# Optimization experiments

Measured on AMD Instinct MI355X. Metric: run time of the kernel, lower is better.

Reference implementation:

```python
import jax, jax.numpy as jnp
import numpy as np

DECAY = 0.99
EPS = 1e-05


def setup_inputs() -> dict:
    key = jax.random.key(0)
    k1, k2 = jax.random.split(key)
    N, D, K = 262144, 32, 1024
    z = jax.random.normal(k1, (N, D), dtype=jnp.float32)
    # xavier_normal_ on (K, D): std = sqrt(2 / (K + D))
    std = float(np.sqrt(2.0 / (K + D)))
    embedding = jax.random.normal(k2, (K, D), dtype=jnp.float32) * std
    embed_avg = embedding  # buffer initialized as a clone of the codebook
    cluster_size = jnp.ones((K,), dtype=jnp.float32)
    return {"z": z, "embedding": embedding, "embed_avg": embed_avg,
            "cluster_size": cluster_size}


def reference(z, embedding, embed_avg, cluster_size):
    n_embed, embed_dim = embedding.shape
    # squared euclidean cdist: ||z||^2 + ||e||^2 - 2 z e^T  -> [N, K]
    d = (jnp.sum(z * z, axis=1, keepdims=True)
         + jnp.sum(embedding * embedding, axis=1)
         - 2.0 * (z @ embedding.T))
    encoding_indices = jnp.argmin(d, axis=1)  # [N]
    # one-hot column sums via scatter-add (counts per code)
    counts = jnp.zeros((n_embed,), z.dtype).at[encoding_indices].add(1.0)
    unused_codes = jnp.sum(counts == 0)
    # embedding gather
    z_q = embedding[encoding_indices]  # [N, D]
    # EMA scatter-add update (training branch, use_ema=True)
    embed_sum = jnp.zeros_like(embedding).at[encoding_indices].add(z)  # [K, D]
    cluster_size_new = DECAY * cluster_size + (1.0 - DECAY) * counts
    embed_avg_new = DECAY * embed_avg + (1.0 - DECAY) * embed_sum
    n = jnp.sum(cluster_size_new)
    norm_w = n * (cluster_size_new + EPS) / (n + n_embed * EPS)  # Laplace smoothing
    embedding_new = embed_avg_new / norm_w[:, None]
    codebook_loss = jnp.float32(0.0)
    commitment_loss = jnp.mean((z - jax.lax.stop_gradient(z_q)) ** 2)
    # straight-through estimator
    z_q_out = z + jax.lax.stop_gradient(z_q - z)
    return (z_q_out, codebook_loss, commitment_loss, encoding_indices,
            unused_codes, embedding_new, cluster_size_new, embed_avg_new)
```

## Files before the change

### kernel.cpp

```cpp
#include <hip/hip_runtime.h>
#include <hip/hip_bf16.h>
#include <float.h>

#define DIM 32
#define KCODES 1024
#define NROWS 262144

#define O_ZQ   0
#define O_CB   8388608
#define O_CL   8388609
#define O_IDX  8388610
#define O_UN   8650754
#define O_EMB  8650755
#define O_CS   8683523
#define O_EA   8684547

#define W_PCNT 0
#define W_PSUM 262144
#define W_PCOM 8650752
#define W_NORM 8651008
#define W_ZZH  8652032
#define W_EEH  8914176
#define W_BF   8915200

typedef __attribute__((ext_vector_type(8))) short bf16x8;
typedef __attribute__((ext_vector_type(4))) float f32x4;

#define MFMA16 __builtin_amdgcn_mfma_f32_16x16x32_bf16

static __device__ __forceinline__ unsigned short f2bf(float x) {
    __hip_bfloat16 h = __float2bfloat16(x);
    return __builtin_bit_cast(unsigned short, h);
}
static __device__ __forceinline__ float bf2f(unsigned short u) {
    unsigned int v = ((unsigned int)u) << 16;
    return __builtin_bit_cast(float, v);
}
static __device__ __forceinline__ float pw8_sq(const float* x) {
    float w[32];
    #pragma unroll
    for (int i = 0; i < 32; ++i) w[i] = __fmul_rn(x[i], x[i]);
    float r[8];
    #pragma unroll
    for (int j = 0; j < 8; ++j) r[j] = ((w[j] + w[8 + j]) + w[16 + j]) + w[24 + j];
    return ((r[0] + r[1]) + (r[2] + r[3])) + ((r[4] + r[5]) + (r[6] + r[7]));
}

__global__ __launch_bounds__(256) void vq_prep_z(
    const float* __restrict__ z, float* __restrict__ ws)
{
    int row = blockIdx.x * 256 + threadIdx.x;
    float x[32];
    const float4* zg = (const float4*)(z + (size_t)row * DIM);
    #pragma unroll
    for (int q = 0; q < 8; ++q) {
        float4 v = zg[q];
        x[4*q] = v.x; x[4*q+1] = v.y; x[4*q+2] = v.z; x[4*q+3] = v.w;
    }
    ws[W_ZZH + row] = 0.5f * pw8_sq(x);
}

__global__ __launch_bounds__(256) void vq_prep_e(
    const float* __restrict__ emb, float* __restrict__ ws)
{
    int c = blockIdx.x * 256 + threadIdx.x;
    float x[32];
    const float4* eg = (const float4*)(emb + (size_t)c * DIM);
    #pragma unroll
    for (int q = 0; q < 8; ++q) {
        float4 v = eg[q];
        x[4*q] = v.x; x[4*q+1] = v.y; x[4*q+2] = v.z; x[4*q+3] = v.w;
    }
    ws[W_EEH + c] = 0.5f * pw8_sq(x);

    unsigned short hb[3][32];
    #pragma unroll
    for (int i = 0; i < 32; ++i) {
        float v = x[i];
        unsigned short h0 = f2bf(v); float f0 = bf2f(h0); float r1 = v - f0;
        unsigned short h1 = f2bf(r1); float f1 = bf2f(h1); float r2 = r1 - f1;
        unsigned short h2 = f2bf(r2);
        hb[0][i] = h0; hb[1][i] = h1; hb[2][i] = h2;
    }
    bf16x8* bf = (bf16x8*)(ws + W_BF);
    int kt = c >> 4, cl = c & 15;
    #pragma unroll
    for (int s = 0; s < 3; ++s) {
        #pragma unroll
        for (int j = 0; j < 4; ++j) {
            bf16x8 pk;
            #pragma unroll
            for (int e = 0; e < 8; ++e) pk[e] = (short)hb[s][j*8 + e];
            bf[(kt*3 + s)*64 + j*16 + cl] = pk;
        }
    }
}

__global__ __launch_bounds__(256, 4) void vq_argmin_mfma(
    const float* __restrict__ z, const float* __restrict__ wsc,
    float* __restrict__ out)
{
    __shared__ float eesh[1024];
    const int t = threadIdx.x;
    const int lane = t & 63, w = t >> 6;
    const int g = lane >> 4, lr = lane & 15;

    const bf16x8* bvG = (const bf16x8*)(wsc + W_BF);

    #pragma unroll
    for (int i = 0; i < 4; ++i) eesh[t + i * 256] = wsc[W_EEH + t + i * 256];

    const int rtbase = blockIdx.x * 16 + w * 4;
    bf16x8 zh[4], zm[4], zl[4];
    float zza[4][4];
    #pragma unroll
    for (int j = 0; j < 4; ++j) {
        const int rtg = rtbase + j;
        const float* zp = z + ((size_t)(rtg * 16 + lr)) * DIM + g * 8;
        float4 a4 = *(const float4*)zp, b4 = *(const float4*)(zp + 4);
        float xs[8] = {a4.x, a4.y, a4.z, a4.w, b4.x, b4.y, b4.z, b4.w};
        #pragma unroll
        for (int e = 0; e < 8; ++e) {
            float v = xs[e];
            unsigned short h0 = f2bf(v); float f0 = bf2f(h0); float r1 = v - f0;
            unsigned short h1 = f2bf(r1); float f1 = bf2f(h1); float r2 = r1 - f1;
            zh[j][e] = (short)h0; zm[j][e] = (short)h1; zl[j][e] = (short)f2bf(r2);
        }
        float4 zv = *(const float4*)(wsc + W_ZZH + rtg * 16 + g * 4);
        zza[j][0] = zv.x; zza[j][1] = zv.y; zza[j][2] = zv.z; zza[j][3] = zv.w;
    }

    unsigned int Bb[4][4]; int Kk[4][4];
    #pragma unroll
    for (int j = 0; j < 4; ++j)
        #pragma unroll
        for (int r = 0; r < 4; ++r) { Bb[j][r] = 0xFFFFFFFFu; Kk[j][r] = 0; }

    __syncthreads();

    #pragma unroll 2
    for (int kt = 0; kt < 64; ++kt) {
        bf16x8 eh = bvG[(kt * 3 + 0) * 64 + lane];
        bf16x8 em = bvG[(kt * 3 + 1) * 64 + lane];
        bf16x8 el = bvG[(kt * 3 + 2) * 64 + lane];
        float ee_l = eesh[kt * 16 + lr];
        int kge = kt * 16 + lr;
        #pragma unroll
        for (int j = 0; j < 4; ++j) {
            f32x4 a = {0.f, 0.f, 0.f, 0.f};
            a = MFMA16(zh[j], eh, a, 0, 0, 0);
            a = MFMA16(zh[j], em, a, 0, 0, 0);
            a = MFMA16(zm[j], eh, a, 0, 0, 0);
            a = MFMA16(zh[j], el, a, 0, 0, 0);
            a = MFMA16(zl[j], eh, a, 0, 0, 0);
            a = MFMA16(zm[j], em, a, 0, 0, 0);
            #pragma unroll
            for (int r = 0; r < 4; ++r) {
                float v = (zza[j][r] + ee_l) - a[r];
                unsigned int u = __builtin_bit_cast(unsigned int, v);
                bool tk = u < Bb[j][r];
                Bb[j][r] = tk ? u : Bb[j][r];
                Kk[j][r] = tk ? kge : Kk[j][r];
            }
        }
    }

    #pragma unroll
    for (int j = 0; j < 4; ++j) {
        const int rtg = rtbase + j;
        #pragma unroll
        for (int r = 0; r < 4; ++r) {
            unsigned int b0 = Bb[j][r]; int k0 = Kk[j][r];
            #pragma unroll
            for (int m = 1; m < 16; m <<= 1) {
                unsigned int ob = __shfl_xor((int)b0, m, 16); int ok = __shfl_xor(k0, m, 16);
                bool tk = (ob < b0) || (ob == b0 && ok < k0);
                b0 = tk ? ob : b0; k0 = tk ? ok : k0;
            }
            if (lr == 0) out[O_IDX + rtg * 16 + g * 4 + r] = (float)k0;
        }
    }
}

__global__ __launch_bounds__(1024) void vq_scatter(
    const float* __restrict__ z, const float* __restrict__ emb,
    float* __restrict__ out, float* __restrict__ ws)
{
    __shared__ float smem[34816];
    __shared__ float red[16];
    const int t = threadIdx.x;
    const int b = blockIdx.x;
    {
        float4 zero4 = {0.f, 0.f, 0.f, 0.f};
        float4* s4 = (float4*)smem;
        #pragma unroll
        for (int i = 0; i < 9; ++i) { int j = t + i * 1024; if (j < 8704) s4[j] = zero4; }
    }
    __syncthreads();

    const int row = b * 1024 + t;
    const int kk = (int)out[O_IDX + row];
    const float4* zg = (const float4*)(z + (size_t)row * DIM);
    const float4* eg = (const float4*)(emb + (size_t)kk * DIM);
    float4* og = (float4*)(out + O_ZQ + (size_t)row * DIM);
    float zv[32];
    float csum = 0.f;
    #pragma unroll
    for (int q = 0; q < 8; ++q) {
        float4 v = zg[q];
        float4 e = eg[q];
        zv[4*q] = v.x; zv[4*q+1] = v.y; zv[4*q+2] = v.z; zv[4*q+3] = v.w;
        float d0 = v.x - e.x, d1 = v.y - e.y, d2 = v.z - e.z, d3 = v.w - e.w;
        csum = fmaf(d0, d0, csum); csum = fmaf(d1, d1, csum);
        csum = fmaf(d2, d2, csum); csum = fmaf(d3, d3, csum);
        float4 o;
        o.x = v.x + (e.x - v.x); o.y = v.y + (e.y - v.y);
        o.z = v.z + (e.z - v.z); o.w = v.w + (e.w - v.w);
        og[q] = o;
    }
    atomicAdd(&smem[33792 + kk], 1.0f);
    #pragma unroll
    for (int i = 0; i < 32; ++i) atomicAdd(&smem[kk * 33 + i], zv[i]);

    #pragma unroll
    for (int off = 32; off > 0; off >>= 1) csum += __shfl_down(csum, off, 64);
    if ((t & 63) == 0) red[t >> 6] = csum;
    __syncthreads();

    float cpart = smem[33792 + t];
    if (cpart != 0.f) atomicAdd(&ws[W_PCNT + t], cpart);

    float4* p4 = (float4*)(ws + W_PSUM + (size_t)b * (KCODES * DIM));
    #pragma unroll
    for (int c = 0; c < 8; ++c) {
        int j = t + c * 1024;
        int kr = j >> 3, e0 = (j & 7) * 4;
        float4 v;
        v.x = smem[kr * 33 + e0 + 0]; v.y = smem[kr * 33 + e0 + 1];
        v.z = smem[kr * 33 + e0 + 2]; v.w = smem[kr * 33 + e0 + 3];
        p4[j] = v;
    }
    if (t == 0) {
        float s = 0.f;
        #pragma unroll
        for (int i = 0; i < 16; ++i) s += red[i];
        ws[W_PCOM + b] = s;
    }
}

__global__ __launch_bounds__(1024) void vq_epilogue0(
    const float* __restrict__ cs_in, const float* __restrict__ ws,
    float* __restrict__ out, float* __restrict__ wsw)
{
    __shared__ float s1[1024], s2[1024];
    const int k = threadIdx.x;
    float c = ws[W_PCNT + k];
    float csn = 0.99f * cs_in[k] + 0.01f * c;
    out[O_CS + k] = csn;
    s1[k] = csn;
    s2[k] = (c == 0.f) ? 1.f : 0.f;
    __syncthreads();
    for (int s = 512; s > 0; s >>= 1) {
        if (k < s) { s1[k] += s1[k + s]; s2[k] += s2[k + s]; }
        __syncthreads();
    }
    float n = s1[0];
    float unused = s2[0];
    wsw[W_NORM + k] = n * (csn + 1e-5f) / (n + 1024.f * 1e-5f);
    __syncthreads();
    s1[k] = (k < 256) ? ws[W_PCOM + k] : 0.f;
    __syncthreads();
    for (int s = 512; s > 0; s >>= 1) {
        if (k < s) s1[k] += s1[k + s];
        __syncthreads();
    }
    if (k == 0) {
        out[O_CB] = 0.f;
        out[O_CL] = s1[0] / 8388608.f;
        out[O_UN] = unused;
    }
}

__global__ void vq_epilogue1(
    const float* __restrict__ ea, const float* __restrict__ ws,
    float* __restrict__ out)
{
    const int id = blockIdx.x * 128 + threadIdx.x;
    float es = 0.f;
    for (int bb = 0; bb < 256; ++bb) es += ws[W_PSUM + (size_t)bb * (KCODES * DIM) + id];
    float ean = 0.99f * ea[id] + 0.01f * es;
    out[O_EA + id] = ean;
    out[O_EMB + id] = ean / ws[W_NORM + (id >> 5)];
}

extern "C" void kernel_launch(void* const* d_in, const int* in_sizes, int n_in,
                              void* d_out, int out_size, void* d_ws, size_t ws_size,
                              hipStream_t stream)
{
    const float* z   = (const float*)d_in[0];
    const float* emb = (const float*)d_in[1];
    const float* ea  = (const float*)d_in[2];
    const float* cs  = (const float*)d_in[3];
    float* out = (float*)d_out;
    float* ws  = (float*)d_ws;

    hipMemsetAsync(ws + W_PCNT, 0, KCODES * sizeof(float), stream);
    vq_prep_z<<<1024, 256, 0, stream>>>(z, ws);
    vq_prep_e<<<4, 256, 0, stream>>>(emb, ws);
    vq_argmin_mfma<<<1024, 256, 0, stream>>>(z, ws, out);
    vq_scatter<<<256, 1024, 0, stream>>>(z, emb, out, ws);
    vq_epilogue0<<<1, 1024, 0, stream>>>(cs, ws, out, ws);
    vq_epilogue1<<<256, 128, 0, stream>>>(ea, ws, out);
}
```

Before: 176.8 us.

## Fuse z-norm into argmin, interleave MFMA chains, halve scatter blocks

Drops the separate z-norm prep kernel and computes each row's half squared norm inside the argmin kernel with cross-lane shuffles, removing one launch and a round trip through global memory. The argmin inner loop now interleaves the four independent MFMA accumulator chains under raised wave priority, and staggers wave start with s_sleep. The scatter kernel processes two rows per thread with 128 blocks, which halves the partial-sum buffer the epilogue must reduce but gives fewer blocks to spread across the GPU. The workspace layout shifts to match.

Result: slower. 246.6 us (+39.5%).

```diff
diff --git a/kernel.cpp b/kernel.cpp
--- a/kernel.cpp
+++ b/kernel.cpp
@@ -18,10 +18,9 @@
 #define W_PCNT 0
 #define W_PSUM 262144
 #define W_PCOM 8650752
-#define W_NORM 8651008
-#define W_ZZH  8652032
-#define W_EEH  8914176
-#define W_BF   8915200
+#define W_NORM 8652800
+#define W_EEH  8653824
+#define W_BF   8654848
 
 typedef __attribute__((ext_vector_type(8))) short bf16x8;
 typedef __attribute__((ext_vector_type(4))) float f32x4;
@@ -44,20 +43,6 @@
     #pragma unroll
     for (int j = 0; j < 8; ++j) r[j] = ((w[j] + w[8 + j]) + w[16 + j]) + w[24 + j];
     return ((r[0] + r[1]) + (r[2] + r[3])) + ((r[4] + r[5]) + (r[6] + r[7]));
-}
-
-__global__ __launch_bounds__(256) void vq_prep_z(
-    const float* __restrict__ z, float* __restrict__ ws)
-{
-    int row = blockIdx.x * 256 + threadIdx.x;
-    float x[32];
-    const float4* zg = (const float4*)(z + (size_t)row * DIM);
-    #pragma unroll
-    for (int q = 0; q < 8; ++q) {
-        float4 v = zg[q];
-        x[4*q] = v.x; x[4*q+1] = v.y; x[4*q+2] = v.z; x[4*q+3] = v.w;
-    }
-    ws[W_ZZH + row] = 0.5f * pw8_sq(x);
 }
 
 __global__ __launch_bounds__(256) void vq_prep_e(
@@ -105,8 +90,6 @@
     const int lane = t & 63, w = t >> 6;
     const int g = lane >> 4, lr = lane & 15;
 
-    const bf16x8* bvG = (const bf16x8*)(wsc + W_BF);
-
     #pragma unroll
     for (int i = 0; i < 4; ++i) eesh[t + i * 256] = wsc[W_EEH + t + i * 256];
 
@@ -119,15 +102,26 @@
         const float* zp = z + ((size_t)(rtg * 16 + lr)) * DIM + g * 8;
         float4 a4 = *(const float4*)zp, b4 = *(const float4*)(zp + 4);
         float xs[8] = {a4.x, a4.y, a4.z, a4.w, b4.x, b4.y, b4.z, b4.w};
+        float r8[8];
         #pragma unroll
         for (int e = 0; e < 8; ++e) {
             float v = xs[e];
             unsigned short h0 = f2bf(v); float f0 = bf2f(h0); float r1 = v - f0;
             unsigned short h1 = f2bf(r1); float f1 = bf2f(h1); float r2 = r1 - f1;
             zh[j][e] = (short)h0; zm[j][e] = (short)h1; zl[j][e] = (short)f2bf(r2);
-        }
-        float4 zv = *(const float4*)(wsc + W_ZZH + rtg * 16 + g * 4);
-        zza[j][0] = zv.x; zza[j][1] = zv.y; zza[j][2] = zv.z; zza[j][3] = zv.w;
+            float wq = __fmul_rn(v, v);
+            float b16 = __shfl_xor(wq, 16);
+            float b32 = __shfl_xor(wq, 32);
+            float b48 = __shfl_xor(wq, 48);
+            float t1 = (g < 2) ? (wq + b16) : (b32 + b48);
+            float c2 = (g == 0) ? b32 : (g == 1) ? b48 : (g == 2) ? wq : b16;
+            float c3 = (g == 0) ? b48 : (g == 1) ? b32 : (g == 2) ? b16 : wq;
+            r8[e] = (t1 + c2) + c3;
+        }
+        float zzf = ((r8[0] + r8[1]) + (r8[2] + r8[3])) + ((r8[4] + r8[5]) + (r8[6] + r8[7]));
+        float zzh2 = 0.5f * zzf;
+        #pragma unroll
+        for (int r = 0; r < 4; ++r) zza[j][r] = __shfl(zzh2, g * 4 + r, 16);
     }
 
     unsigned int Bb[4][4]; int Kk[4][4];
@@ -137,31 +131,61 @@
         for (int r = 0; r < 4; ++r) { Bb[j][r] = 0xFFFFFFFFu; Kk[j][r] = 0; }
 
     __syncthreads();
+
+    for (int i = 0; i < (w & 3); ++i) __builtin_amdgcn_s_sleep(15);
+
+    const char* bp = (const char*)(wsc + W_BF) + (size_t)lane * 16;
 
     #pragma unroll 2
     for (int kt = 0; kt < 64; ++kt) {
-        bf16x8 eh = bvG[(kt * 3 + 0) * 64 + lane];
-        bf16x8 em = bvG[(kt * 3 + 1) * 64 + lane];
-        bf16x8 el = bvG[(kt * 3 + 2) * 64 + lane];
+        const char* pk = bp + (size_t)kt * 3072;
+        bf16x8 eh = *(const bf16x8*)(pk);
+        bf16x8 em = *(const bf16x8*)(pk + 1024);
+        bf16x8 el = *(const bf16x8*)(pk + 2048);
         float ee_l = eesh[kt * 16 + lr];
         int kge = kt * 16 + lr;
-        #pragma unroll
-        for (int j = 0; j < 4; ++j) {
-            f32x4 a = {0.f, 0.f, 0.f, 0.f};
-            a = MFMA16(zh[j], eh, a, 0, 0, 0);
-            a = MFMA16(zh[j], em, a, 0, 0, 0);
-            a = MFMA16(zm[j], eh, a, 0, 0, 0);
-            a = MFMA16(zh[j], el, a, 0, 0, 0);
-            a = MFMA16(zl[j], eh, a, 0, 0, 0);
-            a = MFMA16(zm[j], em, a, 0, 0, 0);
-            #pragma unroll
-            for (int r = 0; r < 4; ++r) {
-                float v = (zza[j][r] + ee_l) - a[r];
-                unsigned int u = __builtin_bit_cast(unsigned int, v);
-                bool tk = u < Bb[j][r];
-                Bb[j][r] = tk ? u : Bb[j][r];
-                Kk[j][r] = tk ? kge : Kk[j][r];
-            }
+        f32x4 aj0 = {0.f,0.f,0.f,0.f}, aj1 = {0.f,0.f,0.f,0.f};
+        f32x4 aj2 = {0.f,0.f,0.f,0.f}, aj3 = {0.f,0.f,0.f,0.f};
+        __builtin_amdgcn_s_setprio(1);
+        aj0 = MFMA16(zh[0], eh, aj0, 0,0,0);
+        aj1 = MFMA16(zh[1], eh, aj1, 0,0,0);
+        aj2 = MFMA16(zh[2], eh, aj2, 0,0,0);
+        aj3 = MFMA16(zh[3], eh, aj3, 0,0,0);
+        aj0 = MFMA16(zh[0], em, aj0, 0,0,0);
+        aj1 = MFMA16(zh[1], em, aj1, 0,0,0);
+        aj2 = MFMA16(zh[2], em, aj2, 0,0,0);
+        aj3 = MFMA16(zh[3], em, aj3, 0,0,0);
+        aj0 = MFMA16(zm[0], eh, aj0, 0,0,0);
+        aj1 = MFMA16(zm[1], eh, aj1, 0,0,0);
+        aj2 = MFMA16(zm[2], eh, aj2, 0,0,0);
+        aj3 = MFMA16(zm[3], eh, aj3, 0,0,0);
+        aj0 = MFMA16(zh[0], el, aj0, 0,0,0);
+        aj1 = MFMA16(zh[1], el, aj1, 0,0,0);
+        aj2 = MFMA16(zh[2], el, aj2, 0,0,0);
+        aj3 = MFMA16(zh[3], el, aj3, 0,0,0);
+        aj0 = MFMA16(zl[0], eh, aj0, 0,0,0);
+        aj1 = MFMA16(zl[1], eh, aj1, 0,0,0);
+        aj2 = MFMA16(zl[2], eh, aj2, 0,0,0);
+        aj3 = MFMA16(zl[3], eh, aj3, 0,0,0);
+        aj0 = MFMA16(zm[0], em, aj0, 0,0,0);
+        aj1 = MFMA16(zm[1], em, aj1, 0,0,0);
+        aj2 = MFMA16(zm[2], em, aj2, 0,0,0);
+        aj3 = MFMA16(zm[3], em, aj3, 0,0,0);
+        __builtin_amdgcn_s_setprio(0);
+        #pragma unroll
+        for (int r = 0; r < 4; ++r) {
+            float v0 = (zza[0][r] + ee_l) - aj0[r];
+            float v1 = (zza[1][r] + ee_l) - aj1[r];
+            float v2 = (zza[2][r] + ee_l) - aj2[r];
+            float v3 = (zza[3][r] + ee_l) - aj3[r];
+            unsigned int u0 = __builtin_bit_cast(unsigned int, v0);
+            unsigned int u1 = __builtin_bit_cast(unsigned int, v1);
+            unsigned int u2 = __builtin_bit_cast(unsigned int, v2);
+            unsigned int u3 = __builtin_bit_cast(unsigned int, v3);
+            bool t0 = u0 < Bb[0][r]; Bb[0][r] = t0 ? u0 : Bb[0][r]; Kk[0][r] = t0 ? kge : Kk[0][r];
+            bool t1 = u1 < Bb[1][r]; Bb[1][r] = t1 ? u1 : Bb[1][r]; Kk[1][r] = t1 ? kge : Kk[1][r];
+            bool t2 = u2 < Bb[2][r]; Bb[2][r] = t2 ? u2 : Bb[2][r]; Kk[2][r] = t2 ? kge : Kk[2][r];
+            bool t3 = u3 < Bb[3][r]; Bb[3][r] = t3 ? u3 : Bb[3][r]; Kk[3][r] = t3 ? kge : Kk[3][r];
         }
     }
 
@@ -198,29 +222,32 @@
     }
     __syncthreads();
 
-    const int row = b * 1024 + t;
-    const int kk = (int)out[O_IDX + row];
-    const float4* zg = (const float4*)(z + (size_t)row * DIM);
-    const float4* eg = (const float4*)(emb + (size_t)kk * DIM);
-    float4* og = (float4*)(out + O_ZQ + (size_t)row * DIM);
-    float zv[32];
     float csum = 0.f;
     #pragma unroll
-    for (int q = 0; q < 8; ++q) {
-        float4 v = zg[q];
-        float4 e = eg[q];
-        zv[4*q] = v.x; zv[4*q+1] = v.y; zv[4*q+2] = v.z; zv[4*q+3] = v.w;
-        float d0 = v.x - e.x, d1 = v.y - e.y, d2 = v.z - e.z, d3 = v.w - e.w;
-        csum = fmaf(d0, d0, csum); csum = fmaf(d1, d1, csum);
-        csum = fmaf(d2, d2, csum); csum = fmaf(d3, d3, csum);
-        float4 o;
-        o.x = v.x + (e.x - v.x); o.y = v.y + (e.y - v.y);
-        o.z = v.z + (e.z - v.z); o.w = v.w + (e.w - v.w);
-        og[q] = o;
-    }
-    atomicAdd(&smem[33792 + kk], 1.0f);
-    #pragma unroll
-    for (int i = 0; i < 32; ++i) atomicAdd(&smem[kk * 33 + i], zv[i]);
+    for (int rr = 0; rr < 2; ++rr) {
+        const int row = b * 2048 + rr * 1024 + t;
+        const int kk = (int)out[O_IDX + row];
+        const float4* zg = (const float4*)(z + (size_t)row * DIM);
+        const float4* eg = (const float4*)(emb + (size_t)kk * DIM);
+        float4* og = (float4*)(out + O_ZQ + (size_t)row * DIM);
+        atomicAdd(&smem[33792 + kk], 1.0f);
+        #pragma unroll
+        for (int q = 0; q < 8; ++q) {
+            float4 v = zg[q];
+            float4 e = eg[q];
+            float d0 = v.x - e.x, d1 = v.y - e.y, d2 = v.z - e.z, d3 = v.w - e.w;
+            csum = fmaf(d0, d0, csum); csum = fmaf(d1, d1, csum);
+            csum = fmaf(d2, d2, csum); csum = fmaf(d3, d3, csum);
+            float4 o;
+            o.x = v.x + (e.x - v.x); o.y = v.y + (e.y - v.y);
+            o.z = v.z + (e.z - v.z); o.w = v.w + (e.w - v.w);
+            og[q] = o;
+            atomicAdd(&smem[kk * 33 + 4 * q + 0], v.x);
+            atomicAdd(&smem[kk * 33 + 4 * q + 1], v.y);
+            atomicAdd(&smem[kk * 33 + 4 * q + 2], v.z);
+            atomicAdd(&smem[kk * 33 + 4 * q + 3], v.w);
+        }
+    }
 
     #pragma unroll
     for (int off = 32; off > 0; off >>= 1) csum += __shfl_down(csum, off, 64);
@@ -268,7 +295,7 @@
     float unused = s2[0];
     wsw[W_NORM + k] = n * (csn + 1e-5f) / (n + 1024.f * 1e-5f);
     __syncthreads();
-    s1[k] = (k < 256) ? ws[W_PCOM + k] : 0.f;
+    s1[k] = (k < 128) ? ws[W_PCOM + k] : 0.f;
     __syncthreads();
     for (int s = 512; s > 0; s >>= 1) {
         if (k < s) s1[k] += s1[k + s];
@@ -287,7 +314,7 @@
 {
     const int id = blockIdx.x * 128 + threadIdx.x;
     float es = 0.f;
-    for (int bb = 0; bb < 256; ++bb) es += ws[W_PSUM + (size_t)bb * (KCODES * DIM) + id];
+    for (int bb = 0; bb < 128; ++bb) es += ws[W_PSUM + (size_t)bb * (KCODES * DIM) + id];
     float ean = 0.99f * ea[id] + 0.01f * es;
     out[O_EA + id] = ean;
     out[O_EMB + id] = ean / ws[W_NORM + (id >> 5)];
@@ -305,10 +332,9 @@
     float* ws  = (float*)d_ws;
 
     hipMemsetAsync(ws + W_PCNT, 0, KCODES * sizeof(float), stream);
-    vq_prep_z<<<1024, 256, 0, stream>>>(z, ws);
     vq_prep_e<<<4, 256, 0, stream>>>(emb, ws);
     vq_argmin_mfma<<<1024, 256, 0, stream>>>(z, ws, out);
-    vq_scatter<<<256, 1024, 0, stream>>>(z, emb, out, ws);
+    vq_scatter<<<128, 1024, 0, stream>>>(z, emb, out, ws);
     vq_epilogue0<<<1, 1024, 0, stream>>>(cs, ws, out, ws);
     vq_epilogue1<<<256, 128, 0, stream>>>(ea, ws, out);
 }
```
